# Kernel optimization log

Hardware: AMD Instinct MI355X
Metric: run time of the kernel (lower is better)

The kernel has to match this reference:

```python
import jax, jax.numpy as jnp
import numpy as np

GAMMA = 0.5
SCALE_BASE = 512.0
LN_EPS = 1e-5


def _xpos(x, downscale=False):
    # x: (B, S, Dh); RetNet XPOS rotary embedding (Jamie-Stirling impl)
    S, Dh = x.shape[1], x.shape[2]
    half = Dh // 2
    base_scale = (jnp.arange(0, Dh, 2, dtype=jnp.float32) + 0.4 * Dh) / (1.4 * Dh)  # (half,)
    power = jnp.arange(S, dtype=jnp.float32)[:, None] / SCALE_BASE                   # (S,1)
    scale = base_scale[None, :] ** power                                             # (S,half)
    inv_freq = 1.0 / (10000.0 ** (jnp.arange(half, dtype=jnp.float32) / half))       # (half,)
    sinusoid = jnp.arange(S, dtype=jnp.float32)[:, None] * inv_freq[None, :]         # (S,half)
    sin, cos = jnp.sin(sinusoid), jnp.cos(sinusoid)
    if downscale:
        scale = 1.0 / scale
    # duplicate_interleave: (S,half) -> (S,Dh) repeating each column twice
    sin_s = jnp.repeat(sin * scale, 2, axis=-1)
    cos_s = jnp.repeat(cos * scale, 2, axis=-1)
    x1, x2 = x[..., ::2], x[..., 1::2]
    rot = jnp.stack((-x2, x1), axis=-1).reshape(x.shape)  # rotate_every_two
    return x * cos_s + rot * sin_s


def _decay_mask(S):
    n = jnp.arange(S)
    diff = (n[:, None] - n[None, :]).astype(jnp.float32)
    return jnp.where(n[:, None] >= n[None, :], GAMMA ** diff, 0.0)  # (S,S)


def setup_inputs() -> dict:
    key = jax.random.key(0)
    ks = jax.random.split(key, 10)
    D, d = 768, 192
    hw, b, s = 196, 8, 32
    x = jax.random.normal(ks[0], (hw, b * s, D), dtype=jnp.float32)
    scale_in = 1.0 / np.sqrt(D)
    scale_d = 1.0 / np.sqrt(d)
    return {
        "x": x,
        "W1": jax.random.normal(ks[1], (D, d), dtype=jnp.float32) * scale_in,
        "b1": jnp.zeros((d,), dtype=jnp.float32),
        "W2": jax.random.normal(ks[2], (d, D), dtype=jnp.float32) * scale_d,
        "b2": jnp.zeros((D,), dtype=jnp.float32),
        "ln_g": jnp.ones((d,), dtype=jnp.float32),
        "ln_b": jnp.zeros((d,), dtype=jnp.float32),
        "WQ": jax.random.normal(ks[3], (d, d), dtype=jnp.float32) * scale_d,
        "WK": jax.random.normal(ks[4], (d, d), dtype=jnp.float32) * scale_d,
        "WV": jax.random.normal(ks[5], (d, d), dtype=jnp.float32) * scale_d,
        "batch_dim": 8,
        "seq_dim": 32,
        "hw": 196,
    }


def reference(x, W1, b1, W2, b2, ln_g, ln_b, WQ, WK, WV, batch_dim, seq_dim, hw):
    D = x.shape[-1]
    # (hw, b*s, D) -> (b*hw, s, D)
    xr = x.reshape(hw, batch_dim, seq_dim, D).transpose(1, 0, 2, 3)
    xr = xr.reshape(batch_dim * hw, seq_dim, D)
    x_down = xr @ W1 + b1  # (B, s, d)
    # LayerNorm
    mu = jnp.mean(x_down, axis=-1, keepdims=True)
    var = jnp.mean((x_down - mu) ** 2, axis=-1, keepdims=True)
    h = (x_down - mu) / jnp.sqrt(var + LN_EPS) * ln_g + ln_b
    # SimpleRetention (parallel form)
    Q = _xpos(h @ WQ, downscale=False)
    K = _xpos(h @ WK, downscale=True)
    V = h @ WV
    Dmask = _decay_mask(seq_dim)  # (s,s)
    att = jnp.einsum("bnd,bmd->bnm", Q, K) * Dmask[None]
    ret = att @ V  # (B, s, d)
    out = xr + (ret @ W2 + b2)
    # (b*hw, s, D) -> (hw, b*s, D)
    out = out.reshape(batch_dim, hw, seq_dim, D).transpose(1, 0, 2, 3)
    return out.reshape(hw, batch_dim * seq_dim, D)
```

## Files before the change

kernel.cpp:

```cpp
#include <hip/hip_runtime.h>

typedef __bf16 bf16x8 __attribute__((ext_vector_type(8)));
typedef __bf16 bf16x4 __attribute__((ext_vector_type(4)));
typedef float floatx4 __attribute__((ext_vector_type(4)));

__device__ __forceinline__ __bf16 f2bf(float f) {
  union { float f; unsigned u; } x; x.f = f;
  unsigned r = (x.u + 0x7FFFu + ((x.u >> 16) & 1u)) >> 16;
  union { unsigned short u; __bf16 b; } o; o.u = (unsigned short)r; return o.b;
}
__device__ __forceinline__ float bf2f(__bf16 b) {
  union { unsigned short u; __bf16 b; } i; i.b = b;
  union { unsigned u; float f; } y; y.u = ((unsigned)i.u) << 16; return y.f;
}

#define MFMA16(a, b, c) __builtin_amdgcn_mfma_f32_16x16x32_bf16(a, b, c, 0, 0, 0)

__global__ __launch_bounds__(256) void prep_weights(
    const float* __restrict__ W1, const float* __restrict__ WQ,
    const float* __restrict__ WK, const float* __restrict__ WV,
    const float* __restrict__ W2,
    __bf16* __restrict__ w1t, __bf16* __restrict__ wqt,
    __bf16* __restrict__ wkt, __bf16* __restrict__ wvt,
    __bf16* __restrict__ w2t) {
  int i = blockIdx.x * 256 + threadIdx.x;
  if (i < 147456) { int n = i / 768, k = i % 768; w1t[i] = f2bf(W1[k * 192 + n]); return; }
  i -= 147456;
  if (i < 36864) { int n = i / 192, k = i % 192; wqt[i] = f2bf(WQ[k * 192 + n]); return; }
  i -= 36864;
  if (i < 36864) { int n = i / 192, k = i % 192; wkt[i] = f2bf(WK[k * 192 + n]); return; }
  i -= 36864;
  if (i < 36864) { int n = i / 192, k = i % 192; wvt[i] = f2bf(WV[k * 192 + n]); return; }
  i -= 36864;
  if (i < 147456) { int n = i / 192, k = i % 192; w2t[i] = f2bf(W2[k * 768 + n]); return; }
}

__global__ __launch_bounds__(256) void prep_tables(
    float* __restrict__ cq, float* __restrict__ sq,
    float* __restrict__ ck, float* __restrict__ sk) {
  int i = blockIdx.x * 256 + threadIdx.x;
  if (i >= 32 * 96) return;
  int s = i / 96, f = i % 96;
  float base = (2.f * f + 0.4f * 192.f) / (1.4f * 192.f);
  float scale = powf(base, (float)s / 512.f);
  float invf = powf(10000.f, -(float)f / 96.f);
  float ang = (float)s * invf;
  float sn = sinf(ang), cs = cosf(ang);
  int o = s * 192 + 2 * f;
  cq[o] = cs * scale; cq[o + 1] = cs * scale;
  sq[o] = sn * scale; sq[o + 1] = sn * scale;
  ck[o] = cs / scale; ck[o + 1] = cs / scale;
  sk[o] = sn / scale; sk[o + 1] = sn / scale;
}

__global__ __launch_bounds__(256, 2) void retnet_main(
    const float* __restrict__ x, const float* __restrict__ b1,
    const float* __restrict__ b2, const float* __restrict__ ln_g,
    const float* __restrict__ ln_b,
    const __bf16* __restrict__ w1t, const __bf16* __restrict__ wqt,
    const __bf16* __restrict__ wkt, const __bf16* __restrict__ wvt,
    const __bf16* __restrict__ w2t,
    const float* __restrict__ cq, const float* __restrict__ sq,
    const float* __restrict__ ck, const float* __restrict__ sk,
    float* __restrict__ out) {
  __shared__ __align__(16) char smem[63488];
  __bf16* A = (__bf16*)smem;
  __bf16* Q = A;
  __bf16* Kl = A + 6144;
  __bf16* Vt = A + 12288;
  __bf16* ret = A + 18432;
  __bf16* h = (__bf16*)(smem + 49152);
  __bf16* att = (__bf16*)(smem + 61440);

  const int tid = threadIdx.x;
  const int wv = tid >> 6;
  const int lane = tid & 63;
  const int l16 = lane & 15;
  const int quad = lane >> 4;
  const int kof = quad * 8;
  const int p = blockIdx.x;
  const float* xblk = x + (size_t)p * 32 * 768;

#pragma unroll 6
  for (int i = 0; i < 24; ++i) {
    int q4 = i * 256 + tid;
    float4 v = ((const float4*)xblk)[q4];
    bf16x4 b; b[0] = f2bf(v.x); b[1] = f2bf(v.y); b[2] = f2bf(v.z); b[3] = f2bf(v.w);
    *(bf16x4*)(A + q4 * 4) = b;
  }
  __syncthreads();

  {
    floatx4 acc[2][3] = {};
#pragma unroll 4
    for (int kk = 0; kk < 768; kk += 32) {
      bf16x8 a0 = *(const bf16x8*)(A + l16 * 768 + kk + kof);
      bf16x8 a1 = *(const bf16x8*)(A + (16 + l16) * 768 + kk + kof);
#pragma unroll
      for (int t = 0; t < 3; ++t) {
        bf16x8 bb = *(const bf16x8*)(w1t + (size_t)(wv * 48 + t * 16 + l16) * 768 + kk + kof);
        acc[0][t] = MFMA16(a0, bb, acc[0][t]);
        acc[1][t] = MFMA16(a1, bb, acc[1][t]);
      }
    }
#pragma unroll
    for (int m = 0; m < 2; ++m)
#pragma unroll
      for (int t = 0; t < 3; ++t) {
        int col = wv * 48 + t * 16 + l16;
        float bias = b1[col];
#pragma unroll
        for (int r = 0; r < 4; ++r) {
          int row = m * 16 + quad * 4 + r;
          h[row * 192 + col] = f2bf(acc[m][t][r] + bias);
        }
      }
  }
  __syncthreads();

  {
    int r = tid >> 3, g = tid & 7;
    float vals[24]; float s = 0.f, s2 = 0.f;
#pragma unroll
    for (int j = 0; j < 24; ++j) {
      float v = bf2f(h[r * 192 + g * 24 + j]);
      vals[j] = v; s += v; s2 += v * v;
    }
#pragma unroll
    for (int o = 1; o < 8; o <<= 1) { s += __shfl_xor(s, o); s2 += __shfl_xor(s2, o); }
    float mu = s * (1.f / 192.f);
    float var = s2 * (1.f / 192.f) - mu * mu;
    float rstd = rsqrtf(var + 1e-5f);
#pragma unroll
    for (int j = 0; j < 24; ++j) {
      int c = g * 24 + j;
      h[r * 192 + c] = f2bf((vals[j] - mu) * rstd * ln_g[c] + ln_b[c]);
    }
  }
  __syncthreads();

  auto gemm_h = [&](const __bf16* __restrict__ W, floatx4 (&acc)[2][3]) {
#pragma unroll
    for (int kk = 0; kk < 192; kk += 32) {
      bf16x8 a0 = *(const bf16x8*)(h + l16 * 192 + kk + kof);
      bf16x8 a1 = *(const bf16x8*)(h + (16 + l16) * 192 + kk + kof);
#pragma unroll
      for (int t = 0; t < 3; ++t) {
        bf16x8 bb = *(const bf16x8*)(W + (size_t)(wv * 48 + t * 16 + l16) * 192 + kk + kof);
        acc[0][t] = MFMA16(a0, bb, acc[0][t]);
        acc[1][t] = MFMA16(a1, bb, acc[1][t]);
      }
    }
  };
  {
    floatx4 acc[2][3] = {};
    gemm_h(wqt, acc);
#pragma unroll
    for (int m = 0; m < 2; ++m)
#pragma unroll
      for (int t = 0; t < 3; ++t) {
        int col = wv * 48 + t * 16 + l16;
#pragma unroll
        for (int r = 0; r < 4; ++r) {
          int row = m * 16 + quad * 4 + r;
          float v = acc[m][t][r];
          float pr = __shfl_xor(v, 1);
          float o = v * cq[row * 192 + col] + ((lane & 1) ? pr : -pr) * sq[row * 192 + col];
          Q[row * 192 + col] = f2bf(o);
        }
      }
  }
  {
    floatx4 acc[2][3] = {};
    gemm_h(wkt, acc);
#pragma unroll
    for (int m = 0; m < 2; ++m)
#pragma unroll
      for (int t = 0; t < 3; ++t) {
        int col = wv * 48 + t * 16 + l16;
#pragma unroll
        for (int r = 0; r < 4; ++r) {
          int row = m * 16 + quad * 4 + r;
          float v = acc[m][t][r];
          float pr = __shfl_xor(v, 1);
          float o = v * ck[row * 192 + col] + ((lane & 1) ? pr : -pr) * sk[row * 192 + col];
          Kl[row * 192 + col] = f2bf(o);
        }
      }
  }
  {
    floatx4 acc[2][3] = {};
    gemm_h(wvt, acc);
#pragma unroll
    for (int m = 0; m < 2; ++m)
#pragma unroll
      for (int t = 0; t < 3; ++t) {
        int col = wv * 48 + t * 16 + l16;
        int s0 = m * 16 + quad * 4;
        bf16x4 pk;
#pragma unroll
        for (int r = 0; r < 4; ++r) pk[r] = f2bf(acc[m][t][r]);
        *(bf16x4*)(Vt + col * 32 + s0) = pk;
      }
  }
  __syncthreads();

  {
    int mt = wv >> 1, nt = wv & 1;
    floatx4 acc = {0.f, 0.f, 0.f, 0.f};
#pragma unroll
    for (int kk = 0; kk < 192; kk += 32) {
      bf16x8 a = *(const bf16x8*)(Q + (mt * 16 + l16) * 192 + kk + kof);
      bf16x8 bb = *(const bf16x8*)(Kl + (nt * 16 + l16) * 192 + kk + kof);
      acc = MFMA16(a, bb, acc);
    }
#pragma unroll
    for (int r = 0; r < 4; ++r) {
      int i = mt * 16 + quad * 4 + r;
      int j = nt * 16 + l16;
      float v = (i >= j) ? acc[r] * exp2f((float)(j - i)) : 0.f;
      att[i * 32 + j] = f2bf(v);
    }
  }
  __syncthreads();

  {
    floatx4 acc[2][3] = {};
    bf16x8 a0 = *(const bf16x8*)(att + l16 * 32 + kof);
    bf16x8 a1 = *(const bf16x8*)(att + (16 + l16) * 32 + kof);
#pragma unroll
    for (int t = 0; t < 3; ++t) {
      bf16x8 bb = *(const bf16x8*)(Vt + (wv * 48 + t * 16 + l16) * 32 + kof);
      acc[0][t] = MFMA16(a0, bb, acc[0][t]);
      acc[1][t] = MFMA16(a1, bb, acc[1][t]);
    }
#pragma unroll
    for (int m = 0; m < 2; ++m)
#pragma unroll
      for (int t = 0; t < 3; ++t) {
        int col = wv * 48 + t * 16 + l16;
#pragma unroll
        for (int r = 0; r < 4; ++r) {
          int row = m * 16 + quad * 4 + r;
          ret[row * 192 + col] = f2bf(acc[m][t][r]);
        }
      }
  }
  __syncthreads();

  {
    bf16x8 af[2][6];
#pragma unroll
    for (int k6 = 0; k6 < 6; ++k6) {
      af[0][k6] = *(const bf16x8*)(ret + l16 * 192 + k6 * 32 + kof);
      af[1][k6] = *(const bf16x8*)(ret + (16 + l16) * 192 + k6 * 32 + kof);
    }
#pragma unroll
    for (int g = 0; g < 4; ++g) {
      floatx4 acc[2][3] = {};
#pragma unroll
      for (int k6 = 0; k6 < 6; ++k6) {
#pragma unroll
        for (int t = 0; t < 3; ++t) {
          bf16x8 bb = *(const bf16x8*)(w2t + (size_t)(wv * 192 + g * 48 + t * 16 + l16) * 192 + k6 * 32 + kof);
          acc[0][t] = MFMA16(af[0][k6], bb, acc[0][t]);
          acc[1][t] = MFMA16(af[1][k6], bb, acc[1][t]);
        }
      }
#pragma unroll
      for (int m = 0; m < 2; ++m)
#pragma unroll
        for (int t = 0; t < 3; ++t) {
          int col = wv * 192 + g * 48 + t * 16 + l16;
          float bias = b2[col];
#pragma unroll
          for (int r = 0; r < 4; ++r) {
            int row = m * 16 + quad * 4 + r;
            size_t gi = (size_t)p * 24576 + row * 768 + col;
            out[gi] = xblk[row * 768 + col] + acc[m][t][r] + bias;
          }
        }
    }
  }
}

extern "C" void kernel_launch(void* const* d_in, const int* in_sizes, int n_in,
                              void* d_out, int out_size, void* d_ws, size_t ws_size,
                              hipStream_t stream) {
  const float* x = (const float*)d_in[0];
  const float* W1 = (const float*)d_in[1];
  const float* b1 = (const float*)d_in[2];
  const float* W2 = (const float*)d_in[3];
  const float* b2 = (const float*)d_in[4];
  const float* lng = (const float*)d_in[5];
  const float* lnb = (const float*)d_in[6];
  const float* WQ = (const float*)d_in[7];
  const float* WK = (const float*)d_in[8];
  const float* WV = (const float*)d_in[9];
  float* out = (float*)d_out;

  char* ws = (char*)d_ws;
  __bf16* w1t = (__bf16*)(ws + 0);
  __bf16* wqt = (__bf16*)(ws + 294912);
  __bf16* wkt = (__bf16*)(ws + 368640);
  __bf16* wvt = (__bf16*)(ws + 442368);
  __bf16* w2t = (__bf16*)(ws + 516096);
  float* cq = (float*)(ws + 811008);
  float* sq = cq + 6144;
  float* ck = sq + 6144;
  float* sk = ck + 6144;

  hipLaunchKernelGGL(prep_weights, dim3(1584), dim3(256), 0, stream,
                     W1, WQ, WK, WV, W2, w1t, wqt, wkt, wvt, w2t);
  hipLaunchKernelGGL(prep_tables, dim3(12), dim3(256), 0, stream, cq, sq, ck, sk);
  hipLaunchKernelGGL(retnet_main, dim3(1568), dim3(256), 0, stream,
                     x, b1, b2, lng, lnb, w1t, wqt, wkt, wvt, w2t, cq, sq, ck, sk, out);
}
```

Measured before the change: 472.6 us.

## Use 8 waves per block, load x directly, swizzle LDS, shrink shared memory

Blocks grow from 4 to 8 waves, with each wave owning one 16-row M tile instead of two, which halves accumulator registers per wave. The x tile is no longer staged into LDS; each wave reads fp32 rows from global memory and converts them to bf16 in registers. This cuts shared memory from about 62KB to 51KB so more blocks may fit per CU. An XOR swizzle on the h/Q/K buffers and padded strides for Vt and att aim to reduce LDS bank conflicts. In exchange, each W1 B-fragment is now loaded by both M-waves, and the QK^T stage leaves half the waves idle.

```diff
diff --git a/kernel.cpp b/kernel.cpp
--- a/kernel.cpp
+++ b/kernel.cpp
@@ -53,7 +53,9 @@
   sk[o] = sn / scale; sk[o + 1] = sn / scale;
 }
 
-__global__ __launch_bounds__(256, 2) void retnet_main(
+#define SW(r, c) ((r) * 192 + ((c) ^ (((r) & 7) << 3)))
+
+__global__ __launch_bounds__(512, 6) void retnet_main(
     const float* __restrict__ x, const float* __restrict__ b1,
     const float* __restrict__ b2, const float* __restrict__ ln_g,
     const float* __restrict__ ln_b,
@@ -63,14 +65,12 @@
     const float* __restrict__ cq, const float* __restrict__ sq,
     const float* __restrict__ ck, const float* __restrict__ sk,
     float* __restrict__ out) {
-  __shared__ __align__(16) char smem[63488];
-  __bf16* A = (__bf16*)smem;
-  __bf16* Q = A;
-  __bf16* Kl = A + 6144;
-  __bf16* Vt = A + 12288;
-  __bf16* ret = A + 18432;
-  __bf16* h = (__bf16*)(smem + 49152);
-  __bf16* att = (__bf16*)(smem + 61440);
+  __shared__ __align__(16) char smem[52224];
+  __bf16* Q = (__bf16*)smem;
+  __bf16* Kl = (__bf16*)(smem + 12288);
+  __bf16* Vt = (__bf16*)(smem + 24576);
+  __bf16* h = (__bf16*)(smem + 39936);
+  __bf16* att = (__bf16*)smem;
 
   const int tid = threadIdx.x;
   const int wv = tid >> 6;
@@ -78,52 +78,47 @@
   const int l16 = lane & 15;
   const int quad = lane >> 4;
   const int kof = quad * 8;
+  const int wm = wv >> 2;
+  const int wn = wv & 3;
   const int p = blockIdx.x;
   const float* xblk = x + (size_t)p * 32 * 768;
 
-#pragma unroll 6
-  for (int i = 0; i < 24; ++i) {
-    int q4 = i * 256 + tid;
-    float4 v = ((const float4*)xblk)[q4];
-    bf16x4 b; b[0] = f2bf(v.x); b[1] = f2bf(v.y); b[2] = f2bf(v.z); b[3] = f2bf(v.w);
-    *(bf16x4*)(A + q4 * 4) = b;
-  }
-  __syncthreads();
-
-  {
-    floatx4 acc[2][3] = {};
-#pragma unroll 4
+  {
+    floatx4 acc[3] = {};
+    const float* arow = xblk + (wm * 16 + l16) * 768;
+#pragma unroll 2
     for (int kk = 0; kk < 768; kk += 32) {
-      bf16x8 a0 = *(const bf16x8*)(A + l16 * 768 + kk + kof);
-      bf16x8 a1 = *(const bf16x8*)(A + (16 + l16) * 768 + kk + kof);
+      float4 f0 = *(const float4*)(arow + kk + kof);
+      float4 f1 = *(const float4*)(arow + kk + kof + 4);
+      bf16x8 a;
+      a[0] = f2bf(f0.x); a[1] = f2bf(f0.y); a[2] = f2bf(f0.z); a[3] = f2bf(f0.w);
+      a[4] = f2bf(f1.x); a[5] = f2bf(f1.y); a[6] = f2bf(f1.z); a[7] = f2bf(f1.w);
 #pragma unroll
       for (int t = 0; t < 3; ++t) {
-        bf16x8 bb = *(const bf16x8*)(w1t + (size_t)(wv * 48 + t * 16 + l16) * 768 + kk + kof);
-        acc[0][t] = MFMA16(a0, bb, acc[0][t]);
-        acc[1][t] = MFMA16(a1, bb, acc[1][t]);
-      }
-    }
-#pragma unroll
-    for (int m = 0; m < 2; ++m)
-#pragma unroll
-      for (int t = 0; t < 3; ++t) {
-        int col = wv * 48 + t * 16 + l16;
-        float bias = b1[col];
-#pragma unroll
-        for (int r = 0; r < 4; ++r) {
-          int row = m * 16 + quad * 4 + r;
-          h[row * 192 + col] = f2bf(acc[m][t][r] + bias);
-        }
-      }
-  }
-  __syncthreads();
-
-  {
+        bf16x8 bb = *(const bf16x8*)(w1t + (size_t)(wn * 48 + t * 16 + l16) * 768 + kk + kof);
+        acc[t] = MFMA16(a, bb, acc[t]);
+      }
+    }
+#pragma unroll
+    for (int t = 0; t < 3; ++t) {
+      int col = wn * 48 + t * 16 + l16;
+      float bias = b1[col];
+#pragma unroll
+      for (int r = 0; r < 4; ++r) {
+        int row = wm * 16 + quad * 4 + r;
+        h[SW(row, col)] = f2bf(acc[t][r] + bias);
+      }
+    }
+  }
+  __syncthreads();
+
+  if (tid < 256) {
     int r = tid >> 3, g = tid & 7;
     float vals[24]; float s = 0.f, s2 = 0.f;
 #pragma unroll
     for (int j = 0; j < 24; ++j) {
-      float v = bf2f(h[r * 192 + g * 24 + j]);
+      int c = g * 24 + j;
+      float v = bf2f(h[SW(r, c)]);
       vals[j] = v; s += v; s2 += v * v;
     }
 #pragma unroll
@@ -134,152 +129,138 @@
 #pragma unroll
     for (int j = 0; j < 24; ++j) {
       int c = g * 24 + j;
-      h[r * 192 + c] = f2bf((vals[j] - mu) * rstd * ln_g[c] + ln_b[c]);
-    }
-  }
-  __syncthreads();
-
-  auto gemm_h = [&](const __bf16* __restrict__ W, floatx4 (&acc)[2][3]) {
+      h[SW(r, c)] = f2bf((vals[j] - mu) * rstd * ln_g[c] + ln_b[c]);
+    }
+  }
+  __syncthreads();
+
+  auto gemm_h = [&](const __bf16* __restrict__ W, floatx4 (&acc)[3]) {
 #pragma unroll
     for (int kk = 0; kk < 192; kk += 32) {
-      bf16x8 a0 = *(const bf16x8*)(h + l16 * 192 + kk + kof);
-      bf16x8 a1 = *(const bf16x8*)(h + (16 + l16) * 192 + kk + kof);
+      bf16x8 a = *(const bf16x8*)(h + SW(wm * 16 + l16, kk + kof));
 #pragma unroll
       for (int t = 0; t < 3; ++t) {
-        bf16x8 bb = *(const bf16x8*)(W + (size_t)(wv * 48 + t * 16 + l16) * 192 + kk + kof);
-        acc[0][t] = MFMA16(a0, bb, acc[0][t]);
-        acc[1][t] = MFMA16(a1, bb, acc[1][t]);
+        bf16x8 bb = *(const bf16x8*)(W + (size_t)(wn * 48 + t * 16 + l16) * 192 + kk + kof);
+        acc[t] = MFMA16(a, bb, acc[t]);
       }
     }
   };
   {
-    floatx4 acc[2][3] = {};
+    floatx4 acc[3] = {};
     gemm_h(wqt, acc);
 #pragma unroll
-    for (int m = 0; m < 2; ++m)
-#pragma unroll
-      for (int t = 0; t < 3; ++t) {
-        int col = wv * 48 + t * 16 + l16;
-#pragma unroll
-        for (int r = 0; r < 4; ++r) {
-          int row = m * 16 + quad * 4 + r;
-          float v = acc[m][t][r];
-          float pr = __shfl_xor(v, 1);
-          float o = v * cq[row * 192 + col] + ((lane & 1) ? pr : -pr) * sq[row * 192 + col];
-          Q[row * 192 + col] = f2bf(o);
-        }
-      }
-  }
-  {
-    floatx4 acc[2][3] = {};
+    for (int t = 0; t < 3; ++t) {
+      int col = wn * 48 + t * 16 + l16;
+#pragma unroll
+      for (int r = 0; r < 4; ++r) {
+        int row = wm * 16 + quad * 4 + r;
+        float v = acc[t][r];
+        float pr = __shfl_xor(v, 1);
+        float o = v * cq[row * 192 + col] + ((lane & 1) ? pr : -pr) * sq[row * 192 + col];
+        Q[SW(row, col)] = f2bf(o);
+      }
+    }
+  }
+  {
+    floatx4 acc[3] = {};
     gemm_h(wkt, acc);
 #pragma unroll
-    for (int m = 0; m < 2; ++m)
-#pragma unroll
-      for (int t = 0; t < 3; ++t) {
-        int col = wv * 48 + t * 16 + l16;
-#pragma unroll
-        for (int r = 0; r < 4; ++r) {
-          int row = m * 16 + quad * 4 + r;
-          float v = acc[m][t][r];
-          float pr = __shfl_xor(v, 1);
-          float o = v * ck[row * 192 + col] + ((lane & 1) ? pr : -pr) * sk[row * 192 + col];
-          Kl[row * 192 + col] = f2bf(o);
-        }
-      }
-  }
-  {
-    floatx4 acc[2][3] = {};
+    for (int t = 0; t < 3; ++t) {
+      int col = wn * 48 + t * 16 + l16;
+#pragma unroll
+      for (int r = 0; r < 4; ++r) {
+        int row = wm * 16 + quad * 4 + r;
+        float v = acc[t][r];
+        float pr = __shfl_xor(v, 1);
+        float o = v * ck[row * 192 + col] + ((lane & 1) ? pr : -pr) * sk[row * 192 + col];
+        Kl[SW(row, col)] = f2bf(o);
+      }
+    }
+  }
+  {
+    floatx4 acc[3] = {};
     gemm_h(wvt, acc);
 #pragma unroll
-    for (int m = 0; m < 2; ++m)
-#pragma unroll
-      for (int t = 0; t < 3; ++t) {
-        int col = wv * 48 + t * 16 + l16;
-        int s0 = m * 16 + quad * 4;
-        bf16x4 pk;
-#pragma unroll
-        for (int r = 0; r < 4; ++r) pk[r] = f2bf(acc[m][t][r]);
-        *(bf16x4*)(Vt + col * 32 + s0) = pk;
-      }
-  }
-  __syncthreads();
-
-  {
-    int mt = wv >> 1, nt = wv & 1;
-    floatx4 acc = {0.f, 0.f, 0.f, 0.f};
+    for (int t = 0; t < 3; ++t) {
+      int col = wn * 48 + t * 16 + l16;
+      bf16x4 pk;
+#pragma unroll
+      for (int r = 0; r < 4; ++r) pk[r] = f2bf(acc[t][r]);
+      *(bf16x4*)(Vt + col * 40 + wm * 16 + quad * 4) = pk;
+    }
+  }
+  __syncthreads();
+
+  floatx4 acc4 = {0.f, 0.f, 0.f, 0.f};
+  const int mt = wv >> 1, nt = wv & 1;
+  if (wv < 4) {
 #pragma unroll
     for (int kk = 0; kk < 192; kk += 32) {
-      bf16x8 a = *(const bf16x8*)(Q + (mt * 16 + l16) * 192 + kk + kof);
-      bf16x8 bb = *(const bf16x8*)(Kl + (nt * 16 + l16) * 192 + kk + kof);
-      acc = MFMA16(a, bb, acc);
-    }
+      bf16x8 a = *(const bf16x8*)(Q + SW(mt * 16 + l16, kk + kof));
+      bf16x8 bb = *(const bf16x8*)(Kl + SW(nt * 16 + l16, kk + kof));
+      acc4 = MFMA16(a, bb, acc4);
+    }
+  }
+  __syncthreads();
+  if (wv < 4) {
 #pragma unroll
     for (int r = 0; r < 4; ++r) {
       int i = mt * 16 + quad * 4 + r;
       int j = nt * 16 + l16;
-      float v = (i >= j) ? acc[r] * exp2f((float)(j - i)) : 0.f;
-      att[i * 32 + j] = f2bf(v);
-    }
-  }
-  __syncthreads();
-
-  {
-    floatx4 acc[2][3] = {};
-    bf16x8 a0 = *(const bf16x8*)(att + l16 * 32 + kof);
-    bf16x8 a1 = *(const bf16x8*)(att + (16 + l16) * 32 + kof);
-#pragma unroll
-    for (int t = 0; t < 3; ++t) {
-      bf16x8 bb = *(const bf16x8*)(Vt + (wv * 48 + t * 16 + l16) * 32 + kof);
-      acc[0][t] = MFMA16(a0, bb, acc[0][t]);
-      acc[1][t] = MFMA16(a1, bb, acc[1][t]);
-    }
-#pragma unroll
-    for (int m = 0; m < 2; ++m)
+      float v = (i >= j) ? acc4[r] * exp2f((float)(j - i)) : 0.f;
+      att[i * 40 + j] = f2bf(v);
+    }
+  }
+  __syncthreads();
+
+  {
+    floatx4 acc[3] = {};
+    bf16x8 a = *(const bf16x8*)(att + (wm * 16 + l16) * 40 + kof);
+#pragma unroll
+    for (int t = 0; t < 3; ++t) {
+      bf16x8 bb = *(const bf16x8*)(Vt + (wn * 48 + t * 16 + l16) * 40 + kof);
+      acc[t] = MFMA16(a, bb, acc[t]);
+    }
+#pragma unroll
+    for (int t = 0; t < 3; ++t) {
+      int col = wn * 48 + t * 16 + l16;
+#pragma unroll
+      for (int r = 0; r < 4; ++r) {
+        int row = wm * 16 + quad * 4 + r;
+        h[SW(row, col)] = f2bf(acc[t][r]);
+      }
+    }
+  }
+  __syncthreads();
+
+  {
+    bf16x8 af[6];
+    const int arow = wm * 16 + l16;
+#pragma unroll
+    for (int k6 = 0; k6 < 6; ++k6)
+      af[k6] = *(const bf16x8*)(h + SW(arow, k6 * 32 + kof));
+#pragma unroll
+    for (int g = 0; g < 4; ++g) {
+      floatx4 acc[3] = {};
+#pragma unroll
+      for (int k6 = 0; k6 < 6; ++k6) {
+#pragma unroll
+        for (int t = 0; t < 3; ++t) {
+          bf16x8 bb = *(const bf16x8*)(w2t + (size_t)(wn * 192 + g * 48 + t * 16 + l16) * 192 + k6 * 32 + kof);
+          acc[t] = MFMA16(af[k6], bb, acc[t]);
+        }
+      }
 #pragma unroll
       for (int t = 0; t < 3; ++t) {
-        int col = wv * 48 + t * 16 + l16;
+        int col = wn * 192 + g * 48 + t * 16 + l16;
+        float bias = b2[col];
 #pragma unroll
         for (int r = 0; r < 4; ++r) {
-          int row = m * 16 + quad * 4 + r;
-          ret[row * 192 + col] = f2bf(acc[m][t][r]);
+          int row = wm * 16 + quad * 4 + r;
+          size_t gi = (size_t)p * 24576 + row * 768 + col;
+          out[gi] = xblk[row * 768 + col] + acc[t][r] + bias;
         }
       }
-  }
-  __syncthreads();
-
-  {
-    bf16x8 af[2][6];
-#pragma unroll
-    for (int k6 = 0; k6 < 6; ++k6) {
-      af[0][k6] = *(const bf16x8*)(ret + l16 * 192 + k6 * 32 + kof);
-      af[1][k6] = *(const bf16x8*)(ret + (16 + l16) * 192 + k6 * 32 + kof);
-    }
-#pragma unroll
-    for (int g = 0; g < 4; ++g) {
-      floatx4 acc[2][3] = {};
-#pragma unroll
-      for (int k6 = 0; k6 < 6; ++k6) {
-#pragma unroll
-        for (int t = 0; t < 3; ++t) {
-          bf16x8 bb = *(const bf16x8*)(w2t + (size_t)(wv * 192 + g * 48 + t * 16 + l16) * 192 + k6 * 32 + kof);
-          acc[0][t] = MFMA16(af[0][k6], bb, acc[0][t]);
-          acc[1][t] = MFMA16(af[1][k6], bb, acc[1][t]);
-        }
-      }
-#pragma unroll
-      for (int m = 0; m < 2; ++m)
-#pragma unroll
-        for (int t = 0; t < 3; ++t) {
-          int col = wv * 192 + g * 48 + t * 16 + l16;
-          float bias = b2[col];
-#pragma unroll
-          for (int r = 0; r < 4; ++r) {
-            int row = m * 16 + quad * 4 + r;
-            size_t gi = (size_t)p * 24576 + row * 768 + col;
-            out[gi] = xblk[row * 768 + col] + acc[m][t][r] + bias;
-          }
-        }
     }
   }
 }
@@ -313,6 +294,6 @@
   hipLaunchKernelGGL(prep_weights, dim3(1584), dim3(256), 0, stream,
                      W1, WQ, WK, WV, W2, w1t, wqt, wkt, wvt, w2t);
   hipLaunchKernelGGL(prep_tables, dim3(12), dim3(256), 0, stream, cq, sq, ck, sk);
-  hipLaunchKernelGGL(retnet_main, dim3(1568), dim3(256), 0, stream,
+  hipLaunchKernelGGL(retnet_main, dim3(1568), dim3(512), 0, stream,
                      x, b1, b2, lng, lnb, w1t, wqt, wkt, wvt, w2t, cq, sq, ck, sk, out);
 }
```

New measurement: 679.0 us. 43.7% more time.

## Pre-pack weights and x into MFMA fragment order and swizzle shared memory

Applied to the files above, without the earlier changes.

Weights are repacked into per-lane MFMA fragment order so each B-operand load is a contiguous 16-byte-per-lane read. When the workspace is large enough, a separate prep kernel converts x to bf16 in fragment order; otherwise the x tile is read straight from global memory. Shared-memory tiles are XOR-swizzled to avoid bank conflicts, and the footprint shrinks by dropping the A staging buffer and reusing h for the ret output. The separate x pass adds a full extra read of x plus a 77 MB bf16 write and read, which may cost more than it saves.

```diff
diff --git a/kernel.cpp b/kernel.cpp
--- a/kernel.cpp
+++ b/kernel.cpp
@@ -20,19 +20,62 @@
     const float* __restrict__ W1, const float* __restrict__ WQ,
     const float* __restrict__ WK, const float* __restrict__ WV,
     const float* __restrict__ W2,
-    __bf16* __restrict__ w1t, __bf16* __restrict__ wqt,
-    __bf16* __restrict__ wkt, __bf16* __restrict__ wvt,
-    __bf16* __restrict__ w2t) {
+    __bf16* __restrict__ w1f, __bf16* __restrict__ wqf,
+    __bf16* __restrict__ wkf, __bf16* __restrict__ wvf,
+    __bf16* __restrict__ w2f) {
   int i = blockIdx.x * 256 + threadIdx.x;
-  if (i < 147456) { int n = i / 768, k = i % 768; w1t[i] = f2bf(W1[k * 192 + n]); return; }
+  if (i < 147456) {
+    int e = i & 7, lane = (i >> 3) & 63, rest = i >> 9;
+    int kk32 = rest % 24, nt = rest / 24;
+    int n = nt * 16 + (lane & 15), k = kk32 * 32 + (lane >> 4) * 8 + e;
+    w1f[i] = f2bf(W1[k * 192 + n]); return;
+  }
   i -= 147456;
-  if (i < 36864) { int n = i / 192, k = i % 192; wqt[i] = f2bf(WQ[k * 192 + n]); return; }
+  if (i < 36864) {
+    int e = i & 7, lane = (i >> 3) & 63, rest = i >> 9;
+    int kk32 = rest % 6, nt = rest / 6;
+    int n = nt * 16 + (lane & 15), k = kk32 * 32 + (lane >> 4) * 8 + e;
+    wqf[i] = f2bf(WQ[k * 192 + n]); return;
+  }
   i -= 36864;
-  if (i < 36864) { int n = i / 192, k = i % 192; wkt[i] = f2bf(WK[k * 192 + n]); return; }
+  if (i < 36864) {
+    int e = i & 7, lane = (i >> 3) & 63, rest = i >> 9;
+    int kk32 = rest % 6, nt = rest / 6;
+    int n = nt * 16 + (lane & 15), k = kk32 * 32 + (lane >> 4) * 8 + e;
+    wkf[i] = f2bf(WK[k * 192 + n]); return;
+  }
   i -= 36864;
-  if (i < 36864) { int n = i / 192, k = i % 192; wvt[i] = f2bf(WV[k * 192 + n]); return; }
+  if (i < 36864) {
+    int e = i & 7, lane = (i >> 3) & 63, rest = i >> 9;
+    int kk32 = rest % 6, nt = rest / 6;
+    int n = nt * 16 + (lane & 15), k = kk32 * 32 + (lane >> 4) * 8 + e;
+    wvf[i] = f2bf(WV[k * 192 + n]); return;
+  }
   i -= 36864;
-  if (i < 147456) { int n = i / 192, k = i % 192; w2t[i] = f2bf(W2[k * 768 + n]); return; }
+  if (i < 147456) {
+    int e = i & 7, lane = (i >> 3) & 63, rest = i >> 9;
+    int kk32 = rest % 6, nt = rest / 6;
+    int n = nt * 16 + (lane & 15), k = kk32 * 32 + (lane >> 4) * 8 + e;
+    w2f[i] = f2bf(W2[k * 768 + n]); return;
+  }
+}
+
+__global__ __launch_bounds__(256) void prep_xf(
+    const float* __restrict__ x, __bf16* __restrict__ xf) {
+  int j = blockIdx.x * 256 + threadIdx.x;
+  int lane = j & 63;
+  int rest = j >> 6;
+  int kk32 = rest % 24;
+  int rest2 = rest / 24;
+  size_t row = (size_t)rest2 * 16 + (lane & 15);
+  int d = kk32 * 32 + ((lane >> 4) & 3) * 8;
+  const float* src = x + row * 768 + d;
+  float4 f0 = *(const float4*)(src);
+  float4 f1 = *(const float4*)(src + 4);
+  bf16x8 a;
+  a[0] = f2bf(f0.x); a[1] = f2bf(f0.y); a[2] = f2bf(f0.z); a[3] = f2bf(f0.w);
+  a[4] = f2bf(f1.x); a[5] = f2bf(f1.y); a[6] = f2bf(f1.z); a[7] = f2bf(f1.w);
+  *(bf16x8*)(xf + (size_t)j * 8) = a;
 }
 
 __global__ __launch_bounds__(256) void prep_tables(
@@ -53,24 +96,25 @@
   sk[o] = sn / scale; sk[o + 1] = sn / scale;
 }
 
-__global__ __launch_bounds__(256, 2) void retnet_main(
+#define SW(r, c) ((r) * 192 + ((c) ^ (((r) & 7) << 3)))
+
+template <bool USE_XF>
+__global__ __launch_bounds__(256) void retnet_main(
     const float* __restrict__ x, const float* __restrict__ b1,
     const float* __restrict__ b2, const float* __restrict__ ln_g,
     const float* __restrict__ ln_b,
-    const __bf16* __restrict__ w1t, const __bf16* __restrict__ wqt,
-    const __bf16* __restrict__ wkt, const __bf16* __restrict__ wvt,
-    const __bf16* __restrict__ w2t,
+    const __bf16* __restrict__ w1f, const __bf16* __restrict__ wqf,
+    const __bf16* __restrict__ wkf, const __bf16* __restrict__ wvf,
+    const __bf16* __restrict__ w2f,
     const float* __restrict__ cq, const float* __restrict__ sq,
     const float* __restrict__ ck, const float* __restrict__ sk,
-    float* __restrict__ out) {
-  __shared__ __align__(16) char smem[63488];
-  __bf16* A = (__bf16*)smem;
-  __bf16* Q = A;
-  __bf16* Kl = A + 6144;
-  __bf16* Vt = A + 12288;
-  __bf16* ret = A + 18432;
-  __bf16* h = (__bf16*)(smem + 49152);
-  __bf16* att = (__bf16*)(smem + 61440);
+    const __bf16* __restrict__ xf, float* __restrict__ out) {
+  __shared__ __align__(16) char smem[51200];
+  __bf16* Q = (__bf16*)smem;
+  __bf16* Kl = (__bf16*)(smem + 12288);
+  __bf16* Vt = (__bf16*)(smem + 24576);
+  __bf16* att = (__bf16*)(smem + 36864);
+  __bf16* h = (__bf16*)(smem + 38912);
 
   const int tid = threadIdx.x;
   const int wv = tid >> 6;
@@ -81,26 +125,42 @@
   const int p = blockIdx.x;
   const float* xblk = x + (size_t)p * 32 * 768;
 
-#pragma unroll 6
-  for (int i = 0; i < 24; ++i) {
-    int q4 = i * 256 + tid;
-    float4 v = ((const float4*)xblk)[q4];
-    bf16x4 b; b[0] = f2bf(v.x); b[1] = f2bf(v.y); b[2] = f2bf(v.z); b[3] = f2bf(v.w);
-    *(bf16x4*)(A + q4 * 4) = b;
-  }
-  __syncthreads();
-
-  {
-    floatx4 acc[2][3] = {};
+  {
+    floatx4 acc[2][3] = {};
+    if (USE_XF) {
+      const __bf16* xfp = xf + (size_t)p * 24576;
 #pragma unroll 4
-    for (int kk = 0; kk < 768; kk += 32) {
-      bf16x8 a0 = *(const bf16x8*)(A + l16 * 768 + kk + kof);
-      bf16x8 a1 = *(const bf16x8*)(A + (16 + l16) * 768 + kk + kof);
-#pragma unroll
-      for (int t = 0; t < 3; ++t) {
-        bf16x8 bb = *(const bf16x8*)(w1t + (size_t)(wv * 48 + t * 16 + l16) * 768 + kk + kof);
-        acc[0][t] = MFMA16(a0, bb, acc[0][t]);
-        acc[1][t] = MFMA16(a1, bb, acc[1][t]);
+      for (int kk32 = 0; kk32 < 24; ++kk32) {
+        bf16x8 a0 = *(const bf16x8*)(xfp + kk32 * 512 + lane * 8);
+        bf16x8 a1 = *(const bf16x8*)(xfp + 12288 + kk32 * 512 + lane * 8);
+#pragma unroll
+        for (int t = 0; t < 3; ++t) {
+          bf16x8 bb = *(const bf16x8*)(w1f + (size_t)((wv * 3 + t) * 24 + kk32) * 512 + lane * 8);
+          acc[0][t] = MFMA16(a0, bb, acc[0][t]);
+          acc[1][t] = MFMA16(a1, bb, acc[1][t]);
+        }
+      }
+    } else {
+      const float* arow0 = xblk + l16 * 768;
+      const float* arow1 = xblk + (16 + l16) * 768;
+#pragma unroll 2
+      for (int kk = 0; kk < 768; kk += 32) {
+        float4 f0 = *(const float4*)(arow0 + kk + kof);
+        float4 f1 = *(const float4*)(arow0 + kk + kof + 4);
+        float4 g0 = *(const float4*)(arow1 + kk + kof);
+        float4 g1 = *(const float4*)(arow1 + kk + kof + 4);
+        bf16x8 a0, a1;
+        a0[0] = f2bf(f0.x); a0[1] = f2bf(f0.y); a0[2] = f2bf(f0.z); a0[3] = f2bf(f0.w);
+        a0[4] = f2bf(f1.x); a0[5] = f2bf(f1.y); a0[6] = f2bf(f1.z); a0[7] = f2bf(f1.w);
+        a1[0] = f2bf(g0.x); a1[1] = f2bf(g0.y); a1[2] = f2bf(g0.z); a1[3] = f2bf(g0.w);
+        a1[4] = f2bf(g1.x); a1[5] = f2bf(g1.y); a1[6] = f2bf(g1.z); a1[7] = f2bf(g1.w);
+        int kk32 = kk >> 5;
+#pragma unroll
+        for (int t = 0; t < 3; ++t) {
+          bf16x8 bb = *(const bf16x8*)(w1f + (size_t)((wv * 3 + t) * 24 + kk32) * 512 + lane * 8);
+          acc[0][t] = MFMA16(a0, bb, acc[0][t]);
+          acc[1][t] = MFMA16(a1, bb, acc[1][t]);
+        }
       }
     }
 #pragma unroll
@@ -112,7 +172,7 @@
 #pragma unroll
         for (int r = 0; r < 4; ++r) {
           int row = m * 16 + quad * 4 + r;
-          h[row * 192 + col] = f2bf(acc[m][t][r] + bias);
+          h[SW(row, col)] = f2bf(acc[m][t][r] + bias);
         }
       }
   }
@@ -123,7 +183,8 @@
     float vals[24]; float s = 0.f, s2 = 0.f;
 #pragma unroll
     for (int j = 0; j < 24; ++j) {
-      float v = bf2f(h[r * 192 + g * 24 + j]);
+      int c = g * 24 + j;
+      float v = bf2f(h[SW(r, c)]);
       vals[j] = v; s += v; s2 += v * v;
     }
 #pragma unroll
@@ -134,19 +195,19 @@
 #pragma unroll
     for (int j = 0; j < 24; ++j) {
       int c = g * 24 + j;
-      h[r * 192 + c] = f2bf((vals[j] - mu) * rstd * ln_g[c] + ln_b[c]);
-    }
-  }
-  __syncthreads();
-
-  auto gemm_h = [&](const __bf16* __restrict__ W, floatx4 (&acc)[2][3]) {
-#pragma unroll
-    for (int kk = 0; kk < 192; kk += 32) {
-      bf16x8 a0 = *(const bf16x8*)(h + l16 * 192 + kk + kof);
-      bf16x8 a1 = *(const bf16x8*)(h + (16 + l16) * 192 + kk + kof);
-#pragma unroll
-      for (int t = 0; t < 3; ++t) {
-        bf16x8 bb = *(const bf16x8*)(W + (size_t)(wv * 48 + t * 16 + l16) * 192 + kk + kof);
+      h[SW(r, c)] = f2bf((vals[j] - mu) * rstd * ln_g[c] + ln_b[c]);
+    }
+  }
+  __syncthreads();
+
+  auto gemm_h = [&](const __bf16* __restrict__ Wf, floatx4 (&acc)[2][3]) {
+#pragma unroll
+    for (int kk32 = 0; kk32 < 6; ++kk32) {
+      bf16x8 a0 = *(const bf16x8*)(h + SW(l16, kk32 * 32 + kof));
+      bf16x8 a1 = *(const bf16x8*)(h + SW(16 + l16, kk32 * 32 + kof));
+#pragma unroll
+      for (int t = 0; t < 3; ++t) {
+        bf16x8 bb = *(const bf16x8*)(Wf + (size_t)((wv * 3 + t) * 6 + kk32) * 512 + lane * 8);
         acc[0][t] = MFMA16(a0, bb, acc[0][t]);
         acc[1][t] = MFMA16(a1, bb, acc[1][t]);
       }
@@ -154,7 +215,7 @@
   };
   {
     floatx4 acc[2][3] = {};
-    gemm_h(wqt, acc);
+    gemm_h(wqf, acc);
 #pragma unroll
     for (int m = 0; m < 2; ++m)
 #pragma unroll
@@ -166,13 +227,13 @@
           float v = acc[m][t][r];
           float pr = __shfl_xor(v, 1);
           float o = v * cq[row * 192 + col] + ((lane & 1) ? pr : -pr) * sq[row * 192 + col];
-          Q[row * 192 + col] = f2bf(o);
-        }
-      }
-  }
-  {
-    floatx4 acc[2][3] = {};
-    gemm_h(wkt, acc);
+          Q[SW(row, col)] = f2bf(o);
+        }
+      }
+  }
+  {
+    floatx4 acc[2][3] = {};
+    gemm_h(wkf, acc);
 #pragma unroll
     for (int m = 0; m < 2; ++m)
 #pragma unroll
@@ -184,23 +245,22 @@
           float v = acc[m][t][r];
           float pr = __shfl_xor(v, 1);
           float o = v * ck[row * 192 + col] + ((lane & 1) ? pr : -pr) * sk[row * 192 + col];
-          Kl[row * 192 + col] = f2bf(o);
-        }
-      }
-  }
-  {
-    floatx4 acc[2][3] = {};
-    gemm_h(wvt, acc);
-#pragma unroll
-    for (int m = 0; m < 2; ++m)
-#pragma unroll
-      for (int t = 0; t < 3; ++t) {
-        int col = wv * 48 + t * 16 + l16;
-        int s0 = m * 16 + quad * 4;
+          Kl[SW(row, col)] = f2bf(o);
+        }
+      }
+  }
+  {
+    floatx4 acc[2][3] = {};
+    gemm_h(wvf, acc);
+#pragma unroll
+    for (int m = 0; m < 2; ++m)
+#pragma unroll
+      for (int t = 0; t < 3; ++t) {
+        int col = wv * 48 + t * 16 + l16;
         bf16x4 pk;
 #pragma unroll
         for (int r = 0; r < 4; ++r) pk[r] = f2bf(acc[m][t][r]);
-        *(bf16x4*)(Vt + col * 32 + s0) = pk;
+        *(bf16x4*)(Vt + col * 32 + m * 16 + quad * 4) = pk;
       }
   }
   __syncthreads();
@@ -210,8 +270,8 @@
     floatx4 acc = {0.f, 0.f, 0.f, 0.f};
 #pragma unroll
     for (int kk = 0; kk < 192; kk += 32) {
-      bf16x8 a = *(const bf16x8*)(Q + (mt * 16 + l16) * 192 + kk + kof);
-      bf16x8 bb = *(const bf16x8*)(Kl + (nt * 16 + l16) * 192 + kk + kof);
+      bf16x8 a = *(const bf16x8*)(Q + SW(mt * 16 + l16, kk + kof));
+      bf16x8 bb = *(const bf16x8*)(Kl + SW(nt * 16 + l16, kk + kof));
       acc = MFMA16(a, bb, acc);
     }
 #pragma unroll
@@ -242,7 +302,7 @@
 #pragma unroll
         for (int r = 0; r < 4; ++r) {
           int row = m * 16 + quad * 4 + r;
-          ret[row * 192 + col] = f2bf(acc[m][t][r]);
+          h[SW(row, col)] = f2bf(acc[m][t][r]);
         }
       }
   }
@@ -252,8 +312,8 @@
     bf16x8 af[2][6];
 #pragma unroll
     for (int k6 = 0; k6 < 6; ++k6) {
-      af[0][k6] = *(const bf16x8*)(ret + l16 * 192 + k6 * 32 + kof);
-      af[1][k6] = *(const bf16x8*)(ret + (16 + l16) * 192 + k6 * 32 + kof);
+      af[0][k6] = *(const bf16x8*)(h + SW(l16, k6 * 32 + kof));
+      af[1][k6] = *(const bf16x8*)(h + SW(16 + l16, k6 * 32 + kof));
     }
 #pragma unroll
     for (int g = 0; g < 4; ++g) {
@@ -262,7 +322,7 @@
       for (int k6 = 0; k6 < 6; ++k6) {
 #pragma unroll
         for (int t = 0; t < 3; ++t) {
-          bf16x8 bb = *(const bf16x8*)(w2t + (size_t)(wv * 192 + g * 48 + t * 16 + l16) * 192 + k6 * 32 + kof);
+          bf16x8 bb = *(const bf16x8*)(w2f + (size_t)((wv * 12 + g * 3 + t) * 6 + k6) * 512 + lane * 8);
           acc[0][t] = MFMA16(af[0][k6], bb, acc[0][t]);
           acc[1][t] = MFMA16(af[1][k6], bb, acc[1][t]);
         }
@@ -300,19 +360,31 @@
   float* out = (float*)d_out;
 
   char* ws = (char*)d_ws;
-  __bf16* w1t = (__bf16*)(ws + 0);
-  __bf16* wqt = (__bf16*)(ws + 294912);
-  __bf16* wkt = (__bf16*)(ws + 368640);
-  __bf16* wvt = (__bf16*)(ws + 442368);
-  __bf16* w2t = (__bf16*)(ws + 516096);
+  __bf16* w1f = (__bf16*)(ws + 0);
+  __bf16* wqf = (__bf16*)(ws + 294912);
+  __bf16* wkf = (__bf16*)(ws + 368640);
+  __bf16* wvf = (__bf16*)(ws + 442368);
+  __bf16* w2f = (__bf16*)(ws + 516096);
   float* cq = (float*)(ws + 811008);
   float* sq = cq + 6144;
   float* ck = sq + 6144;
   float* sk = ck + 6144;
+  const size_t xf_off = 909312;
+  const size_t xf_bytes = 77070336;
+  bool use_xf = (ws_size >= xf_off + xf_bytes);
+  __bf16* xfp = (__bf16*)(ws + xf_off);
 
   hipLaunchKernelGGL(prep_weights, dim3(1584), dim3(256), 0, stream,
-                     W1, WQ, WK, WV, W2, w1t, wqt, wkt, wvt, w2t);
+                     W1, WQ, WK, WV, W2, w1f, wqf, wkf, wvf, w2f);
   hipLaunchKernelGGL(prep_tables, dim3(12), dim3(256), 0, stream, cq, sq, ck, sk);
-  hipLaunchKernelGGL(retnet_main, dim3(1568), dim3(256), 0, stream,
-                     x, b1, b2, lng, lnb, w1t, wqt, wkt, wvt, w2t, cq, sq, ck, sk, out);
-}
+  if (use_xf) {
+    hipLaunchKernelGGL(prep_xf, dim3(18816), dim3(256), 0, stream, x, xfp);
+    hipLaunchKernelGGL((retnet_main<true>), dim3(1568), dim3(256), 0, stream,
+                       x, b1, b2, lng, lnb, w1f, wqf, wkf, wvf, w2f,
+                       cq, sq, ck, sk, (const __bf16*)xfp, out);
+  } else {
+    hipLaunchKernelGGL((retnet_main<false>), dim3(1568), dim3(256), 0, stream,
+                       x, b1, b2, lng, lnb, w1f, wqf, wkf, wvf, w2f,
+                       cq, sq, ck, sk, (const __bf16*)nullptr, out);
+  }
+}
```

Result: faster. 452.0 us (-4.3%).
